# Kernel optimization log

Hardware: AMD Instinct MI355X
Metric: run time of the kernel (lower is better)

Reference implementation:

```python
import jax, jax.numpy as jnp
import numpy as np

MAXT = 10000
BATCH = 4096
LOG_GAMMA = float(np.log(1.02))
ALPHA = float(np.log(0.99) / 1000.0)
INIT_LOGW = float(np.log(0.248))
INIT_LOGP = float(np.log(0.001))
TEMPERATURE = 1000.0
EPS = 1e-12


def setup_inputs() -> dict:
    key = jax.random.key(0)
    k1, k2 = jax.random.split(key)
    # actions are initialized to -10 in the original module (must be << 0 so exp(a) < 1)
    acts = -10.0 * jnp.ones((MAXT,), dtype=jnp.float32)
    u1 = jax.random.uniform(k1, (MAXT, BATCH), dtype=jnp.float32)
    u2 = jax.random.uniform(k2, (MAXT, BATCH), dtype=jnp.float32)
    return {"acts": acts, "u1": u1, "u2": u2}


def _gumbel_sigmoid(logp, uu1, uu2):
    # logit = logp - log(1 - exp(logp))
    logit = logp - jnp.log1p(-jnp.exp(logp))
    noise = -jnp.log(jnp.log(uu2 + EPS) / jnp.log(uu1 + EPS) + EPS)
    soft = jax.nn.sigmoid(logit + noise)  # gumbel_temp = 1
    hard = (soft > 0.5).astype(soft.dtype)
    # straight-through: hard value, soft gradient
    return soft + jax.lax.stop_gradient(hard - soft)


def reference(acts, u1, u2):
    def step(carry, xs):
        logp, logw, alive, cumrew = carry
        a, uu1, uu2 = xs
        alive = alive * (1.0 - _gumbel_sigmoid(logp, uu1, uu2))
        f = jnp.exp(a)
        new_logw = logw + LOG_GAMMA + jnp.log(1.0 - f)
        new_logp = logp + ALPHA * f * jnp.exp(logw)
        rwd = alive * jnp.exp(new_logw / TEMPERATURE)
        return (new_logp, new_logw, alive, cumrew + rwd), None

    batch = u1.shape[1]
    init = (
        jnp.full((batch,), INIT_LOGP, dtype=jnp.float32),
        jnp.full((batch,), INIT_LOGW, dtype=jnp.float32),
        jnp.ones((batch,), dtype=jnp.float32),
        jnp.zeros((batch,), dtype=jnp.float32),
    )
    (_, _, _, cumrew), _ = jax.lax.scan(step, init, (acts, u1, u2))
    return cumrew.mean()
```

## Files before the change

kernel.cpp:

```cpp
#include <hip/hip_runtime.h>
#include <limits.h>

#define MAXT 10000
#define BATCH 4096
#define NYB 80
#define TCHUNK 16
#define SEGT 1536
#define EPT 6
#define NT2 1024
#define SEG2 10
#define CUT_ODDS 9.3e-13f

#define LOG_GAMMA_C  1.9802627296e-2f
#define ALPHA_C     -1.0050335854e-5f
#define INIT_LOGW_C -1.3943265329f
#define INIT_LOGP_C -6.9077552790f
#define EPS_C        1e-12f

__device__ __forceinline__ float block_exscan_tot(float v, float* sh, int tid,
                                                  int n, float* tot) {
    sh[tid] = v;
    __syncthreads();
    for (int off = 1; off < n; off <<= 1) {
        float x = (tid >= off) ? sh[tid - off] : 0.0f;
        __syncthreads();
        sh[tid] += x;
        __syncthreads();
    }
    float excl = (tid > 0) ? sh[tid - 1] : 0.0f;
    float t_ = sh[n - 1];
    __syncthreads();
    *tot = t_;
    return excl;
}

__global__ __launch_bounds__(256) void scan_fused(
    const float* __restrict__ acts,
    const float* __restrict__ u1, const float* __restrict__ u2,
    unsigned* __restrict__ fftab)
{
    __shared__ float sh[256];
    __shared__ int   shi[256];
    __shared__ float s_gate[SEGT];

    const int tid = threadIdx.x;
    const int b4  = (blockIdx.x * 256 + tid) * 4;
    const float E = EPS_C;

    float carry_w = INIT_LOGW_C;
    float carry_p = INIT_LOGP_C;
    unsigned f0 = MAXT, f1 = MAXT, f2 = MAXT, f3 = MAXT;

    for (int seg_base = 0; seg_base < MAXT; seg_base += SEGT) {
        float fv[EPT], dv[EPT];
        float lsum = 0.0f;
        #pragma unroll
        for (int i = 0; i < EPT; ++i) {
            int t = seg_base + tid * EPT + i;
            if (t < MAXT) {
                float f = expf(acts[t]);
                fv[i] = f;
                dv[i] = LOG_GAMMA_C + logf(1.0f - f);
            } else { fv[i] = 0.0f; dv[i] = 0.0f; }
            lsum += dv[i];
        }
        float dtot;
        float excl = block_exscan_tot(lsum, sh, tid, 256, &dtot);

        float run = carry_w + excl;
        float cv[EPT];
        float csum = 0.0f;
        #pragma unroll
        for (int i = 0; i < EPT; ++i) {
            cv[i] = ALPHA_C * fv[i] * expf(run);
            run += dv[i];
            csum += cv[i];
        }
        float ctot;
        float cexcl = block_exscan_tot(csum, sh, tid, 256, &ctot);

        float logp = carry_p + cexcl;
        int localFirst = INT_MAX;
        #pragma unroll
        for (int i = 0; i < EPT; ++i) {
            int t = seg_base + tid * EPT + i;
            float el   = expf(logp);
            float odds = el / (1.0f - el);
            s_gate[tid * EPT + i] = odds - E;
            if (localFirst == INT_MAX && odds <= CUT_ODDS) localFirst = t;
            logp += cv[i];
        }
        shi[tid] = localFirst;
        __syncthreads();
        for (int off = 128; off > 0; off >>= 1) {
            if (tid < off) shi[tid] = min(shi[tid], shi[tid + off]);
            __syncthreads();
        }
        const int segcut = shi[0];
        __syncthreads();

        const int tlimit = min(segcut, MAXT);
        for (int lc = 0; lc < SEGT / TCHUNK; ++lc) {
            const int cg = seg_base / TCHUNK + lc;
            if ((cg % NYB) != (int)blockIdx.y) continue;
            const int tstart = seg_base + lc * TCHUNK;
            if (tstart >= tlimit) break;
            #pragma unroll
            for (int g = 0; g < TCHUNK / 4; ++g) {
                float4 a[4], c[4];
                float gv[4];
                #pragma unroll
                for (int j = 0; j < 4; ++j) {
                    const int t = tstart + g * 4 + j;
                    a[j]  = *(const float4*)(u1 + (size_t)t * BATCH + b4);
                    c[j]  = *(const float4*)(u2 + (size_t)t * BATCH + b4);
                    gv[j] = s_gate[t - seg_base];
                }
                #pragma unroll
                for (int j = 0; j < 4; ++j) {
                    const unsigned t = (unsigned)(tstart + g * 4 + j);
                    const float k = gv[j];
                    if (__logf(c[j].x + E) > k * __logf(a[j].x + E)) f0 = min(f0, t);
                    if (__logf(c[j].y + E) > k * __logf(a[j].y + E)) f1 = min(f1, t);
                    if (__logf(c[j].z + E) > k * __logf(a[j].z + E)) f2 = min(f2, t);
                    if (__logf(c[j].w + E) > k * __logf(a[j].w + E)) f3 = min(f3, t);
                }
            }
        }

        if (segcut != INT_MAX) break;
        carry_w += dtot;
        carry_p += ctot;
        __syncthreads();
    }

    uint4 outv; outv.x = f0; outv.y = f1; outv.z = f2; outv.w = f3;
    *(uint4*)(fftab + (size_t)blockIdx.y * BATCH + b4) = outv;
}

__global__ __launch_bounds__(NT2) void finalize_kernel(
    const float* __restrict__ acts,
    const unsigned* __restrict__ fftab,
    float* __restrict__ out)
{
    __shared__ float  sh[NT2];
    __shared__ float  rp[MAXT + 1];
    __shared__ double sd[NT2];
    const int tid = threadIdx.x;

    const int t0 = tid * SEG2;
    const int n  = (t0 < MAXT) ? min(SEG2, MAXT - t0) : 0;

    float dv[SEG2];
    float lsum = 0.0f;
    for (int i = 0; i < n; ++i) {
        float f = expf(acts[t0 + i]);
        dv[i] = LOG_GAMMA_C + logf(1.0f - f);
        lsum += dv[i];
    }
    float dtot;
    float excl = block_exscan_tot(lsum, sh, tid, NT2, &dtot);
    float run = INIT_LOGW_C + excl;

    float rv[SEG2];
    float rsum = 0.0f;
    for (int i = 0; i < n; ++i) {
        run += dv[i];
        rv[i] = expf(run * 1e-3f);
        rsum += rv[i];
    }
    float rtot;
    float rexcl = block_exscan_tot(rsum, sh, tid, NT2, &rtot);
    float rrun = rexcl;
    for (int i = 0; i < n; ++i) { rp[t0 + i] = rrun; rrun += rv[i]; }
    if (tid == 0) rp[MAXT] = rtot;
    __syncthreads();

    double s = 0.0;
    for (int b = tid; b < BATCH; b += NT2) {
        unsigned ff = 0xFFFFFFFFu;
        #pragma unroll 8
        for (int y = 0; y < NYB; ++y) ff = min(ff, fftab[(size_t)y * BATCH + b]);
        int t = (int)min(ff, (unsigned)MAXT);
        s += (double)rp[t];
    }
    sd[tid] = s;
    __syncthreads();
    for (int off = NT2 / 2; off > 0; off >>= 1) {
        if (tid < off) sd[tid] += sd[tid + off];
        __syncthreads();
    }
    if (tid == 0) out[0] = (float)(sd[0] / (double)BATCH);
}

extern "C" void kernel_launch(void* const* d_in, const int* in_sizes, int n_in,
                              void* d_out, int out_size, void* d_ws, size_t ws_size,
                              hipStream_t stream) {
    const float* acts = (const float*)d_in[0];
    const float* u1   = (const float*)d_in[1];
    const float* u2   = (const float*)d_in[2];
    float* out = (float*)d_out;

    unsigned* fftab = (unsigned*)d_ws;

    dim3 grid(BATCH / (256 * 4), NYB);
    scan_fused<<<grid, 256, 0, stream>>>(acts, u1, u2, fftab);
    finalize_kernel<<<1, NT2, 0, stream>>>(acts, fftab, out);
}
```

Measured before the change: 291.4 us.

## Fuse finalize into scan kernel with atomics, shuffle scans, and prefetched first chunk

Merges the two kernels into one, using atomicMin into a single per-batch row and a last-block ticket to run the final reduction. This replaces the 80-row table and the separate finalize launch. Block scans now use wave shuffles instead of a shared-memory Hillis-Steele loop, and the first chunk's u1/u2 loads are issued before the scan so their latency overlaps it. The early-exit cut is checked per chunk straight from the gate values rather than through a block-wide min reduction. In exchange it adds two memset launches, atomics, and a serial tail where one block of 256 threads does the finalize work.

```diff
diff --git a/kernel.cpp b/kernel.cpp
--- a/kernel.cpp
+++ b/kernel.cpp
@@ -1,57 +1,94 @@
 #include <hip/hip_runtime.h>
-#include <limits.h>
-
-#define MAXT 10000
-#define BATCH 4096
-#define NYB 80
+
+#define MAXT   10000
+#define BATCH  4096
+#define NXB    4
+#define NYB    80
+#define NBLK   (NXB * NYB)
 #define TCHUNK 16
-#define SEGT 1536
-#define EPT 6
-#define NT2 1024
-#define SEG2 10
-#define CUT_ODDS 9.3e-13f
+#define CHTOT  (MAXT / TCHUNK)
+#define SEGT   1536
+#define EPT    6
+#define CHPS   (SEGT / TCHUNK)
+#define SEGF   40
 
 #define LOG_GAMMA_C  1.9802627296e-2f
 #define ALPHA_C     -1.0050335854e-5f
 #define INIT_LOGW_C -1.3943265329f
 #define INIT_LOGP_C -6.9077552790f
 #define EPS_C        1e-12f
-
-__device__ __forceinline__ float block_exscan_tot(float v, float* sh, int tid,
-                                                  int n, float* tot) {
-    sh[tid] = v;
-    __syncthreads();
-    for (int off = 1; off < n; off <<= 1) {
-        float x = (tid >= off) ? sh[tid - off] : 0.0f;
-        __syncthreads();
-        sh[tid] += x;
-        __syncthreads();
-    }
-    float excl = (tid > 0) ? sh[tid - 1] : 0.0f;
-    float t_ = sh[n - 1];
+#define CUT_GATE    (9.3e-13f - 1e-12f)
+
+__device__ __forceinline__ float wave_inscan(float v, int lane) {
+    #pragma unroll
+    for (int off = 1; off < 64; off <<= 1) {
+        float x = __shfl_up(v, off, 64);
+        if (lane >= off) v += x;
+    }
+    return v;
+}
+
+__device__ __forceinline__ float block_exscan(float v, int tid, float* shw,
+                                              float* tot) {
+    const int lane = tid & 63, wave = tid >> 6;
+    float win = wave_inscan(v, lane);
+    float wex = __shfl_up(win, 1, 64);
+    if (lane == 0) wex = 0.0f;
+    if (lane == 63) shw[wave] = win;
+    __syncthreads();
+    float pre = 0.0f, t_ = 0.0f;
+    #pragma unroll
+    for (int w = 0; w < 4; ++w) {
+        float wt = shw[w];
+        if (w < wave) pre += wt;
+        t_ += wt;
+    }
     __syncthreads();
     *tot = t_;
-    return excl;
-}
-
-__global__ __launch_bounds__(256) void scan_fused(
+    return pre + wex;
+}
+
+__device__ __forceinline__ void gate_test(float4 a, float4 c, unsigned t, float k,
+                                          unsigned& f0, unsigned& f1,
+                                          unsigned& f2, unsigned& f3) {
+    const float E = EPS_C;
+    if (__logf(c.x + E) > k * __logf(a.x + E)) f0 = min(f0, t);
+    if (__logf(c.y + E) > k * __logf(a.y + E)) f1 = min(f1, t);
+    if (__logf(c.z + E) > k * __logf(a.z + E)) f2 = min(f2, t);
+    if (__logf(c.w + E) > k * __logf(a.w + E)) f3 = min(f3, t);
+}
+
+__global__ __launch_bounds__(256, 1) void fused_kernel(
     const float* __restrict__ acts,
     const float* __restrict__ u1, const float* __restrict__ u2,
-    unsigned* __restrict__ fftab)
+    unsigned* __restrict__ ffrow,
+    unsigned* __restrict__ cnt,
+    float* __restrict__ out)
 {
-    __shared__ float sh[256];
-    __shared__ int   shi[256];
-    __shared__ float s_gate[SEGT];
+    __shared__ float    shw[4];
+    __shared__ float    s_gate[SEGT];
+    __shared__ unsigned s_ticket;
+    __shared__ double   sdw[4];
 
     const int tid = threadIdx.x;
+    const int y   = blockIdx.y;
     const int b4  = (blockIdx.x * 256 + tid) * 4;
     const float E = EPS_C;
 
-    float carry_w = INIT_LOGW_C;
-    float carry_p = INIT_LOGP_C;
-    unsigned f0 = MAXT, f1 = MAXT, f2 = MAXT, f3 = MAXT;
-
-    for (int seg_base = 0; seg_base < MAXT; seg_base += SEGT) {
+    const int tpre = TCHUNK * y;
+    float4 pa[TCHUNK], pc[TCHUNK];
+    #pragma unroll
+    for (int j = 0; j < TCHUNK; ++j) {
+        pa[j] = *(const float4*)(u1 + (size_t)(tpre + j) * BATCH + b4);
+        pc[j] = *(const float4*)(u2 + (size_t)(tpre + j) * BATCH + b4);
+    }
+
+    unsigned f0 = ~0u, f1 = ~0u, f2 = ~0u, f3 = ~0u;
+    float carry_w = INIT_LOGW_C, carry_p = INIT_LOGP_C;
+
+    for (int seg = 0; seg * SEGT < MAXT; ++seg) {
+        const int seg_base = seg * SEGT;
+
         float fv[EPT], dv[EPT];
         float lsum = 0.0f;
         #pragma unroll
@@ -65,11 +102,10 @@
             lsum += dv[i];
         }
         float dtot;
-        float excl = block_exscan_tot(lsum, sh, tid, 256, &dtot);
-
-        float run = carry_w + excl;
-        float cv[EPT];
-        float csum = 0.0f;
+        float dex = block_exscan(lsum, tid, shw, &dtot);
+
+        float run = carry_w + dex;
+        float cv[EPT], csum = 0.0f;
         #pragma unroll
         for (int i = 0; i < EPT; ++i) {
             cv[i] = ALPHA_C * fv[i] * expf(run);
@@ -77,120 +113,122 @@
             csum += cv[i];
         }
         float ctot;
-        float cexcl = block_exscan_tot(csum, sh, tid, 256, &ctot);
-
-        float logp = carry_p + cexcl;
-        int localFirst = INT_MAX;
+        float cex = block_exscan(csum, tid, shw, &ctot);
+
+        float logp = carry_p + cex;
         #pragma unroll
         for (int i = 0; i < EPT; ++i) {
-            int t = seg_base + tid * EPT + i;
-            float el   = expf(logp);
+            int idx = tid * EPT + i;
+            int t   = seg_base + idx;
+            float el   = (t < MAXT) ? expf(logp) : 0.0f;
             float odds = el / (1.0f - el);
-            s_gate[tid * EPT + i] = odds - E;
-            if (localFirst == INT_MAX && odds <= CUT_ODDS) localFirst = t;
+            s_gate[idx] = odds - E;
             logp += cv[i];
         }
-        shi[tid] = localFirst;
         __syncthreads();
-        for (int off = 128; off > 0; off >>= 1) {
-            if (tid < off) shi[tid] = min(shi[tid], shi[tid + off]);
-            __syncthreads();
-        }
-        const int segcut = shi[0];
-        __syncthreads();
-
-        const int tlimit = min(segcut, MAXT);
-        for (int lc = 0; lc < SEGT / TCHUNK; ++lc) {
-            const int cg = seg_base / TCHUNK + lc;
-            if ((cg % NYB) != (int)blockIdx.y) continue;
-            const int tstart = seg_base + lc * TCHUNK;
-            if (tstart >= tlimit) break;
-            #pragma unroll
-            for (int g = 0; g < TCHUNK / 4; ++g) {
-                float4 a[4], c[4];
-                float gv[4];
+
+        const int c0 = seg * CHPS, c1 = min(c0 + CHPS, CHTOT);
+        for (int cg = y; cg < CHTOT; cg += NYB) {
+            if (cg < c0) continue;
+            if (cg >= c1) break;
+            const int tstart = cg * TCHUNK;
+            const int idx0   = tstart - seg_base;
+            if (s_gate[idx0] <= CUT_GATE) break;
+            if (cg == y) {
                 #pragma unroll
-                for (int j = 0; j < 4; ++j) {
-                    const int t = tstart + g * 4 + j;
-                    a[j]  = *(const float4*)(u1 + (size_t)t * BATCH + b4);
-                    c[j]  = *(const float4*)(u2 + (size_t)t * BATCH + b4);
-                    gv[j] = s_gate[t - seg_base];
-                }
+                for (int g = 0; g < TCHUNK; ++g)
+                    gate_test(pa[g], pc[g], (unsigned)(tstart + g),
+                              s_gate[idx0 + g], f0, f1, f2, f3);
+            } else {
                 #pragma unroll
-                for (int j = 0; j < 4; ++j) {
-                    const unsigned t = (unsigned)(tstart + g * 4 + j);
-                    const float k = gv[j];
-                    if (__logf(c[j].x + E) > k * __logf(a[j].x + E)) f0 = min(f0, t);
-                    if (__logf(c[j].y + E) > k * __logf(a[j].y + E)) f1 = min(f1, t);
-                    if (__logf(c[j].z + E) > k * __logf(a[j].z + E)) f2 = min(f2, t);
-                    if (__logf(c[j].w + E) > k * __logf(a[j].w + E)) f3 = min(f3, t);
+                for (int q = 0; q < TCHUNK / 4; ++q) {
+                    float4 a[4], c[4];
+                    float gv[4];
+                    #pragma unroll
+                    for (int j = 0; j < 4; ++j) {
+                        const int t = tstart + q * 4 + j;
+                        a[j]  = *(const float4*)(u1 + (size_t)t * BATCH + b4);
+                        c[j]  = *(const float4*)(u2 + (size_t)t * BATCH + b4);
+                        gv[j] = s_gate[idx0 + q * 4 + j];
+                    }
+                    #pragma unroll
+                    for (int j = 0; j < 4; ++j)
+                        gate_test(a[j], c[j], (unsigned)(tstart + q * 4 + j),
+                                  gv[j], f0, f1, f2, f3);
                 }
             }
         }
 
-        if (segcut != INT_MAX) break;
+        if (s_gate[SEGT - 1] <= CUT_GATE) break;
         carry_w += dtot;
         carry_p += ctot;
         __syncthreads();
     }
 
-    uint4 outv; outv.x = f0; outv.y = f1; outv.z = f2; outv.w = f3;
-    *(uint4*)(fftab + (size_t)blockIdx.y * BATCH + b4) = outv;
-}
-
-__global__ __launch_bounds__(NT2) void finalize_kernel(
-    const float* __restrict__ acts,
-    const unsigned* __restrict__ fftab,
-    float* __restrict__ out)
-{
-    __shared__ float  sh[NT2];
-    __shared__ float  rp[MAXT + 1];
-    __shared__ double sd[NT2];
-    const int tid = threadIdx.x;
-
-    const int t0 = tid * SEG2;
-    const int n  = (t0 < MAXT) ? min(SEG2, MAXT - t0) : 0;
-
-    float dv[SEG2];
-    float lsum = 0.0f;
-    for (int i = 0; i < n; ++i) {
-        float f = expf(acts[t0 + i]);
-        dv[i] = LOG_GAMMA_C + logf(1.0f - f);
-        lsum += dv[i];
-    }
-    float dtot;
-    float excl = block_exscan_tot(lsum, sh, tid, NT2, &dtot);
-    float run = INIT_LOGW_C + excl;
-
-    float rv[SEG2];
+    if (f0 != ~0u) atomicMin(ffrow + b4 + 0, f0);
+    if (f1 != ~0u) atomicMin(ffrow + b4 + 1, f1);
+    if (f2 != ~0u) atomicMin(ffrow + b4 + 2, f2);
+    if (f3 != ~0u) atomicMin(ffrow + b4 + 3, f3);
+
+    __syncthreads();
+    if (tid == 0) {
+        __threadfence();
+        s_ticket = atomicAdd(cnt, 1u);
+    }
+    __syncthreads();
+    if (s_ticket != NBLK - 1) return;
+
+    __threadfence();
+    __shared__ float rp[MAXT + 1];
+
+    const int t0 = tid * SEGF;
+    float dvf[SEGF];
+    float dsum = 0.0f;
+    #pragma unroll 8
+    for (int i = 0; i < SEGF; ++i) {
+        int t = t0 + i;
+        if (t < MAXT) {
+            float f = expf(acts[t]);
+            dvf[i] = LOG_GAMMA_C + logf(1.0f - f);
+        } else dvf[i] = 0.0f;
+        dsum += dvf[i];
+    }
+    float dt_;
+    float dex = block_exscan(dsum, tid, shw, &dt_);
+    float run = INIT_LOGW_C + dex;
+
+    float rvf[SEGF];
     float rsum = 0.0f;
-    for (int i = 0; i < n; ++i) {
-        run += dv[i];
-        rv[i] = expf(run * 1e-3f);
-        rsum += rv[i];
+    #pragma unroll 8
+    for (int i = 0; i < SEGF; ++i) {
+        run += dvf[i];
+        rvf[i] = ((t0 + i) < MAXT) ? expf(run * 1e-3f) : 0.0f;
+        rsum += rvf[i];
     }
     float rtot;
-    float rexcl = block_exscan_tot(rsum, sh, tid, NT2, &rtot);
-    float rrun = rexcl;
-    for (int i = 0; i < n; ++i) { rp[t0 + i] = rrun; rrun += rv[i]; }
+    float rex = block_exscan(rsum, tid, shw, &rtot);
+    float rr = rex;
+    #pragma unroll 8
+    for (int i = 0; i < SEGF; ++i) {
+        int t = t0 + i;
+        if (t < MAXT) rp[t] = rr;
+        rr += rvf[i];
+    }
     if (tid == 0) rp[MAXT] = rtot;
     __syncthreads();
 
     double s = 0.0;
-    for (int b = tid; b < BATCH; b += NT2) {
-        unsigned ff = 0xFFFFFFFFu;
-        #pragma unroll 8
-        for (int y = 0; y < NYB; ++y) ff = min(ff, fftab[(size_t)y * BATCH + b]);
-        int t = (int)min(ff, (unsigned)MAXT);
-        s += (double)rp[t];
-    }
-    sd[tid] = s;
-    __syncthreads();
-    for (int off = NT2 / 2; off > 0; off >>= 1) {
-        if (tid < off) sd[tid] += sd[tid + off];
-        __syncthreads();
-    }
-    if (tid == 0) out[0] = (float)(sd[0] / (double)BATCH);
+    for (int b = tid; b < BATCH; b += 256) {
+        unsigned ff = atomicMin(ffrow + b, (unsigned)MAXT);
+        s += (double)rp[min(ff, (unsigned)MAXT)];
+    }
+    const int lane = tid & 63, wave = tid >> 6;
+    #pragma unroll
+    for (int off = 32; off > 0; off >>= 1) s += __shfl_down(s, off, 64);
+    if (lane == 0) sdw[wave] = s;
+    __syncthreads();
+    if (tid == 0)
+        out[0] = (float)((sdw[0] + sdw[1] + sdw[2] + sdw[3]) / (double)BATCH);
 }
 
 extern "C" void kernel_launch(void* const* d_in, const int* in_sizes, int n_in,
@@ -201,9 +239,12 @@
     const float* u2   = (const float*)d_in[2];
     float* out = (float*)d_out;
 
-    unsigned* fftab = (unsigned*)d_ws;
-
-    dim3 grid(BATCH / (256 * 4), NYB);
-    scan_fused<<<grid, 256, 0, stream>>>(acts, u1, u2, fftab);
-    finalize_kernel<<<1, NT2, 0, stream>>>(acts, fftab, out);
-}
+    unsigned* cnt   = (unsigned*)d_ws;
+    unsigned* ffrow = cnt + 64;
+
+    hipMemsetAsync(cnt, 0x00, sizeof(unsigned), stream);
+    hipMemsetAsync(ffrow, 0xFF, BATCH * sizeof(unsigned), stream);
+
+    dim3 grid(NXB, NYB);
+    fused_kernel<<<grid, 256, 0, stream>>>(acts, u1, u2, ffrow, cnt, out);
+}
```

Measured after the change: 319.0 us. 9.5% more time.
